# Kernel tuning notes

Measured on AMD Instinct MI355X. Metric: run time of the kernel, lower is better.

The kernel has to match this reference:

```python
import math
import jax, jax.numpy as jnp
import numpy as np

B, S, H = 8, 1024, 1024
NH = 16
HD = H // NH  # 64


def setup_inputs() -> dict:
    key = jax.random.key(0)
    k1, k2, k3, k4 = jax.random.split(key, 4)
    hidden_states = jax.random.normal(k1, (B, S, H), dtype=jnp.float32)
    attention_mask = jax.random.randint(k2, (B, 1, 1, S), 0, 2, dtype=jnp.int32)
    w_qkv = jax.random.normal(k3, (H, 3 * H), dtype=jnp.float32) * (1.0 / math.sqrt(H))
    b_qkv = jax.random.normal(k4, (3 * H,), dtype=jnp.float32) * 0.02
    return {"hidden_states": hidden_states, "attention_mask": attention_mask,
            "w_qkv": w_qkv, "b_qkv": b_qkv}


def reference(hidden_states, attention_mask, w_qkv, b_qkv):
    b, s, _ = hidden_states.shape
    # fused QKV projection: [b, s, 3H]
    qkv = jnp.einsum('bsh,hk->bsk', hidden_states, w_qkv) + b_qkv
    # view (b, s, nh, 3*hd) -> permute -> chunk last dim (per-head q|k|v layout)
    qkv = qkv.reshape(b, s, NH, 3, HD)
    qkv = jnp.transpose(qkv, (0, 2, 1, 3, 4))      # [b, nh, s, 3, hd]
    q, k, v = qkv[..., 0, :], qkv[..., 1, :], qkv[..., 2, :]
    # raw scores, then FusedScaleMaskSoftmax semantics: scale * scores, mask, fp32 softmax
    scores = jnp.einsum('bhqd,bhkd->bhqk', q, k)
    scale = math.sqrt(HD)  # module passes sqrt(head_dim) as multiplicative scale
    scores = scores.astype(jnp.float32) * scale
    mask = attention_mask != 0                     # nonzero -> masked (padding)
    scores = jnp.where(mask, jnp.float32(-10000.0), scores)
    probs = jax.nn.softmax(scores, axis=-1).astype(hidden_states.dtype)
    # dropout prob = 0 -> identity
    context = jnp.einsum('bhqk,bhkd->bhqd', probs, v)
    context = jnp.transpose(context, (0, 2, 1, 3)).reshape(b, s, NH * HD)
    return context
```

## Files before the change

### kernel.cpp

```cpp
#include <hip/hip_runtime.h>
#include <math.h>

#define Bdim 8
#define Sdim 1024
#define Hdim 1024
#define NHd 16
#define HDd 64
#define N3H 3072

#define Q_OFF   0u
#define K_OFF   16777216u
#define V_OFF   33554432u
#define WH_OFF  41943040u
#define WL_OFF  45088768u
#define AHI_OFF 0u
#define ALO_OFF 8388608u

typedef __bf16 bf16x8 __attribute__((ext_vector_type(8)));
typedef float  f32x4  __attribute__((ext_vector_type(4)));

__device__ __forceinline__ unsigned short f2bf(float x) {
  unsigned b = __builtin_bit_cast(unsigned, x);
  return (unsigned short)((b + 0x7FFFu + ((b >> 16) & 1u)) >> 16);
}
__device__ __forceinline__ float bf2f(unsigned short h) {
  unsigned b = ((unsigned)h) << 16;
  return __builtin_bit_cast(float, b);
}
__device__ __forceinline__ void split_hl(float v, unsigned short& h, unsigned short& l) {
  h = f2bf(v);
  l = f2bf(v - bf2f(h));
}
__device__ __forceinline__ void async16(void* lds, const void* g) {
  __builtin_amdgcn_global_load_lds((const __attribute__((address_space(1))) unsigned int*)g,
                                   (__attribute__((address_space(3))) unsigned int*)lds, 16, 0, 0);
}

template <int CTRL>
__device__ __forceinline__ float dppmax(float v) {
  int x = __builtin_amdgcn_mov_dpp(__builtin_bit_cast(int, v), CTRL, 0xf, 0xf, true);
  return fmaxf(v, __builtin_bit_cast(float, x));
}
__device__ __forceinline__ float rowmax16(float v) {
  v = dppmax<0xB1>(v);
  v = dppmax<0x4E>(v);
  v = dppmax<0x141>(v);
  v = dppmax<0x140>(v);
  return v;
}

__device__ __forceinline__ float exp2g(float x) { return __builtin_amdgcn_exp2f(x); }

__global__ __launch_bounds__(256) void convert_AW(
    const float* __restrict__ A, const float* __restrict__ W,
    unsigned short* __restrict__ aout, unsigned short* __restrict__ ws)
{
  __shared__ float T[64][65];
  const int tid = threadIdx.x;
  int bid = blockIdx.x;
  if (bid < 4096) {
    size_t i = ((size_t)bid * 256 + tid) * 8;
    float4 a0 = *(const float4*)&A[i];
    float4 a1 = *(const float4*)&A[i + 4];
    float av[8] = {a0.x, a0.y, a0.z, a0.w, a1.x, a1.y, a1.z, a1.w};
    unsigned short h[8], l[8];
    #pragma unroll
    for (int j = 0; j < 8; ++j) split_hl(av[j], h[j], l[j]);
    *(uint4*)&aout[AHI_OFF + i] = *(uint4*)h;
    *(uint4*)&aout[ALO_OFF + i] = *(uint4*)l;
    return;
  }
  bid -= 4096;
  const int n0 = (bid % (N3H / 64)) * 64;
  const int k0 = (bid / (N3H / 64)) * 64;
  #pragma unroll
  for (int r = 0; r < 4; ++r) {
    int k = r * 16 + (tid >> 4);
    int n = (tid & 15) * 4;
    float4 v = *(const float4*)&W[(size_t)(k0 + k) * N3H + n0 + n];
    T[k][n + 0] = v.x; T[k][n + 1] = v.y; T[k][n + 2] = v.z; T[k][n + 3] = v.w;
  }
  __syncthreads();
  int n = tid >> 2;
  int kl = (tid & 3) * 16;
  unsigned short h[16], l[16];
  #pragma unroll
  for (int i = 0; i < 16; ++i) split_hl(T[kl + i][n], h[i], l[i]);
  size_t base = (size_t)(n0 + n) * 1024 + k0 + kl;
  *(uint4*)&ws[WH_OFF + base]     = *(uint4*)&h[0];
  *(uint4*)&ws[WH_OFF + base + 8] = *(uint4*)&h[8];
  *(uint4*)&ws[WL_OFF + base]     = *(uint4*)&l[0];
  *(uint4*)&ws[WL_OFF + base + 8] = *(uint4*)&l[8];
}

__global__ __launch_bounds__(256, 2) void qkv_mfma(
    const unsigned short* __restrict__ ao,
    const unsigned short* __restrict__ ws,
    const float* __restrict__ bias,
    unsigned short* __restrict__ wso)
{
  __shared__ unsigned short sA[2][128 * 32];
  __shared__ unsigned short sB[2][128 * 32];

  const int tid  = threadIdx.x;
  const int wave = tid >> 6;
  const int lane = tid & 63;
  const int l16  = lane & 15;
  const int quad = lane >> 4;

  const int n0 = blockIdx.x * 128;
  const int m0 = blockIdx.y * 128;
  const int wm = (wave >> 1) * 64;
  const int wn = (wave & 1) * 64;

  const unsigned short* Ah = ao + AHI_OFF;
  const unsigned short* Al = ao + ALO_OFF;
  const unsigned short* Wh = ws + WH_OFF;
  const unsigned short* Wl = ws + WL_OFF;

  f32x4 acc[4][4];
  #pragma unroll
  for (int i = 0; i < 4; ++i)
    #pragma unroll
    for (int j = 0; j < 4; ++j) acc[i][j] = (f32x4){0.f, 0.f, 0.f, 0.f};

  for (int kt = 0; kt < 1024; kt += 32) {
    __syncthreads();
    #pragma unroll
    for (int r = 0; r < 2; ++r) {
      int chunk = r * 256 + tid;
      int row = chunk >> 2;
      int c8  = (chunk & 3) << 3;
      int ldsoff = (r * 256 + wave * 64) * 8;
      async16(&sA[0][ldsoff], &Ah[(size_t)(m0 + row) * 1024 + kt + c8]);
      async16(&sA[1][ldsoff], &Al[(size_t)(m0 + row) * 1024 + kt + c8]);
      async16(&sB[0][ldsoff], &Wh[(size_t)(n0 + row) * 1024 + kt + c8]);
      async16(&sB[1][ldsoff], &Wl[(size_t)(n0 + row) * 1024 + kt + c8]);
    }
    __syncthreads();

    bf16x8 af[4][2], bf[4][2];
    #pragma unroll
    for (int i = 0; i < 4; ++i) {
      int row = wm + i * 16 + l16;
      af[i][0] = *(const bf16x8*)&sA[0][row * 32 + quad * 8];
      af[i][1] = *(const bf16x8*)&sA[1][row * 32 + quad * 8];
    }
    #pragma unroll
    for (int j = 0; j < 4; ++j) {
      int row = wn + j * 16 + l16;
      bf[j][0] = *(const bf16x8*)&sB[0][row * 32 + quad * 8];
      bf[j][1] = *(const bf16x8*)&sB[1][row * 32 + quad * 8];
    }
    #pragma unroll
    for (int i = 0; i < 4; ++i)
      #pragma unroll
      for (int j = 0; j < 4; ++j) {
        acc[i][j] = __builtin_amdgcn_mfma_f32_16x16x32_bf16(af[i][0], bf[j][0], acc[i][j], 0, 0, 0);
        acc[i][j] = __builtin_amdgcn_mfma_f32_16x16x32_bf16(af[i][1], bf[j][0], acc[i][j], 0, 0, 0);
        acc[i][j] = __builtin_amdgcn_mfma_f32_16x16x32_bf16(af[i][0], bf[j][1], acc[i][j], 0, 0, 0);
      }
  }

  const int ncol0 = n0 + wn;
  const int which = (ncol0 >> 6) % 3;
  const int head  = ncol0 / 192;
  const int mrow0 = m0 + wm;
  const int bb = mrow0 >> 10;
  const int sb = mrow0 & 1023;
  const int bh = bb * NHd + head;

  float bs[4];
  #pragma unroll
  for (int j = 0; j < 4; ++j) bs[j] = bias[ncol0 + j * 16 + l16];

  if (which == 0) {
    unsigned short* dst = wso + Q_OFF + ((size_t)bh * Sdim + sb) * 128;
    #pragma unroll
    for (int i = 0; i < 4; ++i)
      #pragma unroll
      for (int j = 0; j < 4; ++j) {
        int d = j * 16 + l16;
        #pragma unroll
        for (int r = 0; r < 4; ++r) {
          int s = i * 16 + quad * 4 + r;
          unsigned short h, l;
          split_hl(acc[i][j][r] + bs[j], h, l);
          dst[(size_t)s * 128 + d]      = h;
          dst[(size_t)s * 128 + 64 + d] = l;
        }
      }
  } else if (which == 1) {
    unsigned short* dst = wso + K_OFF + (size_t)bh * 131072 + (size_t)(sb >> 6) * 8192;
    #pragma unroll
    for (int i = 0; i < 4; ++i)
      #pragma unroll
      for (int j = 0; j < 4; ++j) {
        int c = j * 16 + l16;
        #pragma unroll
        for (int r = 0; r < 4; ++r) {
          int sp = i * 16 + quad * 4 + r;
          int idx = ((((sp >> 4) * 4 + (c >> 5)) * 64 + ((c >> 3) & 3) * 16 + (sp & 15)) << 3) + (c & 7);
          unsigned short h, l;
          split_hl(acc[i][j][r] + bs[j], h, l);
          dst[idx]        = h;
          dst[idx + 1024] = l;
        }
      }
  } else {
    unsigned short* dst = wso + V_OFF + (size_t)bh * 65536 + (size_t)(sb >> 6) * 4096;
    #pragma unroll
    for (int i = 0; i < 4; ++i)
      #pragma unroll
      for (int j = 0; j < 4; ++j) {
        int dr = j * 16 + l16;
        int ky = i * 16 + quad * 4;
        int idx = ((((dr >> 4) * 2 + (ky >> 5)) * 64 + ((ky >> 3) & 3) * 16 + (dr & 15)) << 3) + (ky & 7);
        unsigned short p[4];
        #pragma unroll
        for (int r = 0; r < 4; ++r) p[r] = f2bf(acc[i][j][r] + bs[j]);
        *(uint2*)&dst[idx] = *(uint2*)p;
      }
  }
}

__global__ __launch_bounds__(256, 3) void attn_mfma(
    const unsigned short* __restrict__ qhl,
    const unsigned short* __restrict__ khl,
    const unsigned short* __restrict__ vt,
    const int* __restrict__ mask,
    float* __restrict__ out)
{
  __shared__ unsigned short Ks[8192];
  __shared__ unsigned short Vs[4096];
  __shared__ unsigned short Pw[4][2048];
  __shared__ unsigned short msks[1024];

  const int tid  = threadIdx.x;
  const int wave = tid >> 6;
  const int lane = tid & 63;
  const int l16  = lane & 15;
  const int quad = lane >> 4;

  const int xcd = blockIdx.x & 7;
  const int s_  = blockIdx.x >> 3;
  const int bh  = xcd + ((s_ & 7) << 3) + ((s_ >> 6) << 6);
  const int qt  = (s_ >> 3) & 7;
  const int bb  = bh >> 4;
  const int q0  = qt * 128;

  const float SCL = 11.5415603f;
  const float MSKV = -14427.0f;

  const unsigned short* kplane = khl + (size_t)bh * 131072;
  const unsigned short* vplane = vt  + (size_t)bh * 65536;

  bf16x8 onesv;
  #pragma unroll
  for (int i = 0; i < 8; ++i) onesv[i] = (__bf16)1.0f;

  {
    int4 mv = *(const int4*)&mask[bb * Sdim + tid * 4];
    msks[tid * 4 + 0] = (unsigned short)(mv.x ? 1 : 0);
    msks[tid * 4 + 1] = (unsigned short)(mv.y ? 1 : 0);
    msks[tid * 4 + 2] = (unsigned short)(mv.z ? 1 : 0);
    msks[tid * 4 + 3] = (unsigned short)(mv.w ? 1 : 0);
  }

  bf16x8 qfA[4], qfB[4];
  {
    int rowA = q0 + wave * 32 + l16;
    const unsigned short* srcA = qhl + ((size_t)bh * Sdim + rowA) * 128;
    const unsigned short* srcB = srcA + 16 * 128;
    #pragma unroll
    for (int kk = 0; kk < 4; ++kk) {
      qfA[kk] = *(const bf16x8*)&srcA[kk * 32 + quad * 8];
      qfB[kk] = *(const bf16x8*)&srcB[kk * 32 + quad * 8];
    }
  }

  f32x4 OA[4] = {{0.f,0.f,0.f,0.f},{0.f,0.f,0.f,0.f},{0.f,0.f,0.f,0.f},{0.f,0.f,0.f,0.f}};
  f32x4 OB[4] = {{0.f,0.f,0.f,0.f},{0.f,0.f,0.f,0.f},{0.f,0.f,0.f,0.f},{0.f,0.f,0.f,0.f}};
  float mrowA[4] = {-INFINITY,-INFINITY,-INFINITY,-INFINITY};
  float mrowB[4] = {-INFINITY,-INFINITY,-INFINITY,-INFINITY};
  float lrowA[4] = {0.f,0.f,0.f,0.f};
  float lrowB[4] = {0.f,0.f,0.f,0.f};

  #pragma unroll 1
  for (int kt = 0; kt < 16; ++kt) {
    __syncthreads();
    {
      const unsigned short* ksrc = kplane + (size_t)kt * 8192;
      const unsigned short* vsrc = vplane + (size_t)kt * 4096;
      #pragma unroll
      for (int r = 0; r < 4; ++r)
        async16(&Ks[(r * 256 + tid) * 8], &ksrc[(size_t)(r * 256 + tid) * 8]);
      #pragma unroll
      for (int r = 0; r < 2; ++r)
        async16(&Vs[(r * 256 + tid) * 8], &vsrc[(size_t)(r * 256 + tid) * 8]);
    }
    __syncthreads();

    f32x4 scA[4], scB[4];
    __builtin_amdgcn_s_setprio(1);
    #pragma unroll
    for (int ns = 0; ns < 4; ++ns) {
      bf16x8 kf0 = *(const bf16x8*)&Ks[((ns * 4 + 0) * 64 + lane) * 8];
      bf16x8 kf1 = *(const bf16x8*)&Ks[((ns * 4 + 1) * 64 + lane) * 8];
      bf16x8 kf2 = *(const bf16x8*)&Ks[((ns * 4 + 2) * 64 + lane) * 8];
      bf16x8 kf3 = *(const bf16x8*)&Ks[((ns * 4 + 3) * 64 + lane) * 8];
      f32x4 cA = {0.f,0.f,0.f,0.f}, cB = {0.f,0.f,0.f,0.f};
      cA = __builtin_amdgcn_mfma_f32_16x16x32_bf16(qfA[0], kf0, cA, 0, 0, 0);
      cB = __builtin_amdgcn_mfma_f32_16x16x32_bf16(qfB[0], kf0, cB, 0, 0, 0);
      cA = __builtin_amdgcn_mfma_f32_16x16x32_bf16(qfA[1], kf1, cA, 0, 0, 0);
      cB = __builtin_amdgcn_mfma_f32_16x16x32_bf16(qfB[1], kf1, cB, 0, 0, 0);
      cA = __builtin_amdgcn_mfma_f32_16x16x32_bf16(qfA[2], kf0, cA, 0, 0, 0);
      cB = __builtin_amdgcn_mfma_f32_16x16x32_bf16(qfB[2], kf0, cB, 0, 0, 0);
      cA = __builtin_amdgcn_mfma_f32_16x16x32_bf16(qfA[3], kf1, cA, 0, 0, 0);
      cB = __builtin_amdgcn_mfma_f32_16x16x32_bf16(qfB[3], kf1, cB, 0, 0, 0);
      cA = __builtin_amdgcn_mfma_f32_16x16x32_bf16(qfA[0], kf2, cA, 0, 0, 0);
      cB = __builtin_amdgcn_mfma_f32_16x16x32_bf16(qfB[0], kf2, cB, 0, 0, 0);
      cA = __builtin_amdgcn_mfma_f32_16x16x32_bf16(qfA[1], kf3, cA, 0, 0, 0);
      cB = __builtin_amdgcn_mfma_f32_16x16x32_bf16(qfB[1], kf3, cB, 0, 0, 0);
      scA[ns] = cA; scB[ns] = cB;
    }
    __builtin_amdgcn_s_setprio(0);

    float rmaxA[4] = {-INFINITY,-INFINITY,-INFINITY,-INFINITY};
    float rmaxB[4] = {-INFINITY,-INFINITY,-INFINITY,-INFINITY};
    #pragma unroll
    for (int ns = 0; ns < 4; ++ns) {
      unsigned short mk = msks[kt * 64 + ns * 16 + l16];
      #pragma unroll
      for (int r = 0; r < 4; ++r) {
        float sA2 = mk ? MSKV : scA[ns][r] * SCL;
        float sB2 = mk ? MSKV : scB[ns][r] * SCL;
        scA[ns][r] = sA2; scB[ns][r] = sB2;
        rmaxA[r] = fmaxf(rmaxA[r], sA2);
        rmaxB[r] = fmaxf(rmaxB[r], sB2);
      }
    }
    #pragma unroll
    for (int r = 0; r < 4; ++r) {
      rmaxA[r] = rowmax16(rmaxA[r]);
      rmaxB[r] = rowmax16(rmaxB[r]);
    }

    bool nosk = !(rmaxA[0] <= mrowA[0] + 8.f && rmaxA[1] <= mrowA[1] + 8.f &&
                  rmaxA[2] <= mrowA[2] + 8.f && rmaxA[3] <= mrowA[3] + 8.f &&
                  rmaxB[0] <= mrowB[0] + 8.f && rmaxB[1] <= mrowB[1] + 8.f &&
                  rmaxB[2] <= mrowB[2] + 8.f && rmaxB[3] <= mrowB[3] + 8.f);
    if (__any((int)nosk)) {
      #pragma unroll
      for (int r = 0; r < 4; ++r) {
        float mnA = fmaxf(mrowA[r], rmaxA[r]);
        float mnB = fmaxf(mrowB[r], rmaxB[r]);
        float aA = exp2g(mrowA[r] - mnA);
        float aB = exp2g(mrowB[r] - mnB);
        mrowA[r] = mnA; mrowB[r] = mnB;
        lrowA[r] *= aA;  lrowB[r] *= aB;
        #pragma unroll
        for (int d = 0; d < 4; ++d) { OA[d][r] *= aA; OB[d][r] *= aB; }
      }
    }

    #pragma unroll
    for (int ns = 0; ns < 4; ++ns) {
      int key = ns * 16 + l16;
      int cbase = (((key >> 5) * 4 + ((key >> 3) & 3)) * 16 + quad * 4) * 8 + (key & 7);
      #pragma unroll
      for (int r = 0; r < 4; ++r) {
        float pA = exp2g(scA[ns][r] - mrowA[r]);
        float pB = exp2g(scB[ns][r] - mrowB[r]);
        Pw[wave][cbase + r * 8]        = __builtin_bit_cast(unsigned short, (__bf16)pA);
        Pw[wave][1024 + cbase + r * 8] = __builtin_bit_cast(unsigned short, (__bf16)pB);
      }
    }

    bf16x8 pfA[2], pfB[2];
    #pragma unroll
    for (int kk = 0; kk < 2; ++kk) {
      pfA[kk] = *(const bf16x8*)&Pw[wave][((kk * 4 + quad) * 16 + l16) * 8];
      pfB[kk] = *(const bf16x8*)&Pw[wave][1024 + ((kk * 4 + quad) * 16 + l16) * 8];
    }
    f32x4 smA = {0.f,0.f,0.f,0.f}, smB = {0.f,0.f,0.f,0.f};
    __builtin_amdgcn_s_setprio(1);
    #pragma unroll
    for (int d = 0; d < 4; ++d)
      #pragma unroll
      for (int kk = 0; kk < 2; ++kk) {
        bf16x8 vf = *(const bf16x8*)&Vs[((d * 2 + kk) * 64 + lane) * 8];
        OA[d] = __builtin_amdgcn_mfma_f32_16x16x32_bf16(pfA[kk], vf, OA[d], 0, 0, 0);
        OB[d] = __builtin_amdgcn_mfma_f32_16x16x32_bf16(pfB[kk], vf, OB[d], 0, 0, 0);
      }
    smA = __builtin_amdgcn_mfma_f32_16x16x32_bf16(pfA[0], onesv, smA, 0, 0, 0);
    smA = __builtin_amdgcn_mfma_f32_16x16x32_bf16(pfA[1], onesv, smA, 0, 0, 0);
    smB = __builtin_amdgcn_mfma_f32_16x16x32_bf16(pfB[0], onesv, smB, 0, 0, 0);
    smB = __builtin_amdgcn_mfma_f32_16x16x32_bf16(pfB[1], onesv, smB, 0, 0, 0);
    __builtin_amdgcn_s_setprio(0);
    #pragma unroll
    for (int r = 0; r < 4; ++r) { lrowA[r] += smA[r]; lrowB[r] += smB[r]; }
  }

  const int h = bh & 15;
  #pragma unroll
  for (int r = 0; r < 4; ++r) {
    float invA = 1.f / lrowA[r];
    float invB = 1.f / lrowB[r];
    int qA = q0 + wave * 32 + quad * 4 + r;
    float* dstA = out + ((size_t)bb * Sdim + qA) * Hdim + h * HDd;
    float* dstB = dstA + 16 * Hdim;
    #pragma unroll
    for (int d = 0; d < 4; ++d) {
      dstA[d * 16 + l16] = OA[d][r] * invA;
      dstB[d * 16 + l16] = OB[d][r] * invB;
    }
  }
}

extern "C" void kernel_launch(void* const* d_in, const int* in_sizes, int n_in,
                              void* d_out, int out_size, void* d_ws, size_t ws_size,
                              hipStream_t stream) {
  const float* hs   = (const float*)d_in[0];
  const int*   mask = (const int*)d_in[1];
  const float* w    = (const float*)d_in[2];
  const float* bias = (const float*)d_in[3];
  float* out = (float*)d_out;
  unsigned short* ws = (unsigned short*)d_ws;
  unsigned short* ao = (unsigned short*)d_out;

  convert_AW<<<4096 + (N3H / 64) * (1024 / 64), 256, 0, stream>>>(hs, w, ao, ws);

  qkv_mfma<<<dim3(N3H / 128, 8192 / 128), 256, 0, stream>>>(ao, ws, bias, ws);

  attn_mfma<<<Bdim * NHd * (Sdim / 128), 256, 0, stream>>>(
      ws + Q_OFF, ws + K_OFF, ws + V_OFF, mask, out);
}
```

Before: 340.6 us.

## Prefetch next K/V tile into registers to overlap global loads with attention compute

Replaces the per-iteration synchronous async16 copies of K and V tiles into LDS with register prefetching. The loads for tile kt+2 are issued into registers while tile kt+1 sits in LDS, so global-memory latency overlaps the MFMA and softmax work of the current iteration. This costs 24 extra VGPRs per thread for the staging registers, which may reduce occupancy, and it adds an extra LDS store pass in place of direct-to-LDS loads.

```diff
diff --git a/kernel.cpp b/kernel.cpp
--- a/kernel.cpp
+++ b/kernel.cpp
@@ -255,9 +255,41 @@
   const unsigned short* kplane = khl + (size_t)bh * 131072;
   const unsigned short* vplane = vt  + (size_t)bh * 65536;
 
+#define BARRIER() do { \
+    asm volatile("s_waitcnt lgkmcnt(0)" ::: "memory"); \
+    __builtin_amdgcn_sched_barrier(0); \
+    __builtin_amdgcn_s_barrier(); \
+    __builtin_amdgcn_sched_barrier(0); \
+  } while (0)
+
+  uint4 kv0, kv1, kv2, kv3, kv4, kv5;
+
+#define KV_ISSUE(t_) do { \
+    int _t = (t_) < 15 ? (t_) : 15; \
+    const unsigned short* _ks = kplane + (size_t)_t * 8192; \
+    const unsigned short* _vs = vplane + (size_t)_t * 4096; \
+    kv0 = *(const uint4*)&_ks[(size_t)(0 * 256 + tid) * 8]; \
+    kv1 = *(const uint4*)&_ks[(size_t)(1 * 256 + tid) * 8]; \
+    kv2 = *(const uint4*)&_ks[(size_t)(2 * 256 + tid) * 8]; \
+    kv3 = *(const uint4*)&_ks[(size_t)(3 * 256 + tid) * 8]; \
+    kv4 = *(const uint4*)&_vs[(size_t)(0 * 256 + tid) * 8]; \
+    kv5 = *(const uint4*)&_vs[(size_t)(1 * 256 + tid) * 8]; \
+  } while (0)
+
+#define KV_WRITE() do { \
+    *(uint4*)&Ks[(0 * 256 + tid) * 8] = kv0; \
+    *(uint4*)&Ks[(1 * 256 + tid) * 8] = kv1; \
+    *(uint4*)&Ks[(2 * 256 + tid) * 8] = kv2; \
+    *(uint4*)&Ks[(3 * 256 + tid) * 8] = kv3; \
+    *(uint4*)&Vs[(0 * 256 + tid) * 8] = kv4; \
+    *(uint4*)&Vs[(1 * 256 + tid) * 8] = kv5; \
+  } while (0)
+
   bf16x8 onesv;
   #pragma unroll
   for (int i = 0; i < 8; ++i) onesv[i] = (__bf16)1.0f;
+
+  KV_ISSUE(0);
 
   {
     int4 mv = *(const int4*)&mask[bb * Sdim + tid * 4];
@@ -279,6 +311,10 @@
     }
   }
 
+  KV_WRITE();
+  KV_ISSUE(1);
+  BARRIER();
+
   f32x4 OA[4] = {{0.f,0.f,0.f,0.f},{0.f,0.f,0.f,0.f},{0.f,0.f,0.f,0.f},{0.f,0.f,0.f,0.f}};
   f32x4 OB[4] = {{0.f,0.f,0.f,0.f},{0.f,0.f,0.f,0.f},{0.f,0.f,0.f,0.f},{0.f,0.f,0.f,0.f}};
   float mrowA[4] = {-INFINITY,-INFINITY,-INFINITY,-INFINITY};
@@ -288,18 +324,6 @@
 
   #pragma unroll 1
   for (int kt = 0; kt < 16; ++kt) {
-    __syncthreads();
-    {
-      const unsigned short* ksrc = kplane + (size_t)kt * 8192;
-      const unsigned short* vsrc = vplane + (size_t)kt * 4096;
-      #pragma unroll
-      for (int r = 0; r < 4; ++r)
-        async16(&Ks[(r * 256 + tid) * 8], &ksrc[(size_t)(r * 256 + tid) * 8]);
-      #pragma unroll
-      for (int r = 0; r < 2; ++r)
-        async16(&Vs[(r * 256 + tid) * 8], &vsrc[(size_t)(r * 256 + tid) * 8]);
-    }
-    __syncthreads();
 
     f32x4 scA[4], scB[4];
     __builtin_amdgcn_s_setprio(1);
@@ -400,6 +424,13 @@
     __builtin_amdgcn_s_setprio(0);
     #pragma unroll
     for (int r = 0; r < 4; ++r) { lrowA[r] += smA[r]; lrowB[r] += smB[r]; }
+
+    BARRIER();
+    if (kt < 15) {
+      KV_WRITE();
+      KV_ISSUE(kt + 2);
+      BARRIER();
+    }
   }
 
   const int h = bh & 15;
@@ -416,6 +447,10 @@
       dstB[d * 16 + l16] = OB[d][r] * invB;
     }
   }
+
+#undef BARRIER
+#undef KV_ISSUE
+#undef KV_WRITE
 }
 
 extern "C" void kernel_launch(void* const* d_in, const int* in_sizes, int n_in,
```

After: 368.4 us. 8.2% more time.
